# Optimization experiments

Measured on AMD Instinct MI355X. Metric: run time of the kernel, lower is better.

The kernel has to match this reference:

```python
import jax, jax.numpy as jnp
from jax import lax
import numpy as np

B, T, K = 256, 1024, 128


def setup_inputs() -> dict:
    key = jax.random.key(0)
    k1, k2, k3 = jax.random.split(key, 3)
    inputs = jax.random.normal(k1, (B, T, K), dtype=jnp.float32)
    transitions = jax.random.normal(k2, (K, K), dtype=jnp.float32)
    tags = jax.random.randint(k3, (B, T), 0, K, dtype=jnp.int64)
    mask = jnp.ones((B, T), dtype=jnp.int32)
    return {"inputs": inputs, "transitions": transitions, "tags": tags, "mask": mask}


def _input_likelihood(inputs, transitions, maskf):
    # inputs: [B,T,K] emissions; forward algorithm (no start/end transitions)
    emit = jnp.transpose(inputs, (1, 0, 2))  # [T,B,K]
    m = jnp.transpose(maskf, (1, 0))         # [T,B]
    alpha0 = emit[0]                          # [B,K]

    def step(alpha, xm):
        e, mi = xm  # e: [B,K], mi: [B]
        # inner[b,i,j] = alpha[b,i] + transitions[i,j] + e[b,j]
        inner = alpha[:, :, None] + transitions[None, :, :] + e[:, None, :]
        new = jax.nn.logsumexp(inner, axis=1)  # [B,K]
        alpha = new * mi[:, None] + alpha * (1.0 - mi[:, None])
        return alpha, None

    alpha, _ = lax.scan(step, alpha0, (emit[1:], m[1:]))
    return jax.nn.logsumexp(alpha, axis=-1)  # [B]


def _joint_likelihood(inputs, transitions, tags, mask, maskf):
    b, t, k = inputs.shape
    # transition scores between consecutive gold tags
    trans_scores = transitions[tags[:, :-1], tags[:, 1:]]              # [B,T-1]
    # emission scores at gold tags
    emit_scores = jnp.take_along_axis(inputs, tags[..., None], axis=2)[..., 0]  # [B,T]
    score = jnp.sum(trans_scores * maskf[:, 1:], axis=-1) \
          + jnp.sum(emit_scores[:, :-1] * maskf[:, :-1], axis=-1)
    # last valid tag's emission at the final timestep (AllenNLP semantics)
    last_idx = jnp.sum(mask, axis=1).astype(jnp.int32) - 1             # [B]
    last_tags = jnp.take_along_axis(tags, last_idx[:, None].astype(tags.dtype), axis=1)[:, 0]
    last_input_score = jnp.take_along_axis(inputs[:, -1, :], last_tags[:, None], axis=1)[:, 0]
    score = score + last_input_score * maskf[:, -1]
    return score  # [B]


def reference(inputs, transitions, tags, mask):
    maskf = mask.astype(inputs.dtype)
    log_denominator = _input_likelihood(inputs, transitions, maskf)
    log_numerator = _joint_likelihood(inputs, transitions, tags, mask, maskf)
    loglik = log_numerator - log_denominator
    return jnp.sum(loglik)  # reduction='sum'
```

## Files before the change

kernel.cpp:

```cpp
#include <hip/hip_runtime.h>
#include <math.h>

#define BB 256
#define TT 1024
#define KK 128
#define NTHR 512
#define CHUNK 16
#define NCHUNK (TT / CHUNK)
#define QSTR 40

__global__ void zero_out_kernel(float* out) { out[0] = 0.0f; }

#define LOBF(u) __uint_as_float((u) << 16)
#define HIBF(u) __uint_as_float((u) & 0xFFFF0000u)

#define LDE(V, I0) { V.x = expf(tcol[(size_t)(I0) * KK]); \
                     V.y = expf(tcol[(size_t)((I0) + 1) * KK]); \
                     V.z = expf(tcol[(size_t)((I0) + 2) * KK]); \
                     V.w = expf(tcol[(size_t)((I0) + 3) * KK]); }

#define FMA8(V, EA, EB) { \
    z0 = fmaf(LOBF(V.x), EA.x, z0); z1 = fmaf(HIBF(V.x), EA.y, z1); \
    z2 = fmaf(LOBF(V.y), EA.z, z2); z3 = fmaf(HIBF(V.y), EA.w, z3); \
    z0 = fmaf(LOBF(V.z), EB.x, z0); z1 = fmaf(HIBF(V.z), EB.y, z1); \
    z2 = fmaf(LOBF(V.w), EB.z, z2); z3 = fmaf(HIBF(V.w), EB.w, z3); }

#define BARSYNC() { asm volatile("s_waitcnt lgkmcnt(0)" ::: "memory"); \
                    __builtin_amdgcn_s_barrier(); \
                    asm volatile("" ::: "memory"); }

__global__ __launch_bounds__(NTHR, 2) void crf_kernel(
    const float* __restrict__ inputs,
    const float* __restrict__ trans,
    const int* __restrict__ tags,
    const int* __restrict__ mask,
    float* __restrict__ out)
{
    __shared__ __align__(16) unsigned short pbuf[2][4 * QSTR];
    __shared__ __align__(16) float ebuf[2][CHUNK * KK];
    __shared__ float mbuf[2][CHUNK];
    __shared__ float scratch[16];

    const int tid = threadIdx.x;
    const int q   = tid & 3;
    const int j   = tid >> 2;
    const int b   = blockIdx.x;

    const float* binp = inputs + (size_t)b * TT * KK;
    const int* bmask  = mask + (size_t)b * TT;
    const int* btags  = tags + (size_t)b * TT;

    const float* tcol = trans + j;
    const int ib = q * 32;
    float4 E0, E1, E2, E3, E4, E5, E6, E7;
    LDE(E0, ib + 0)  LDE(E1, ib + 4)
    LDE(E2, ib + 8)  LDE(E3, ib + 12)
    LDE(E4, ib + 16) LDE(E5, ib + 20)
    LDE(E6, ib + 24) LDE(E7, ib + 28)

    {
        float4 e4 = ((const float4*)binp)[tid];
        e4.x = __expf(e4.x); e4.y = __expf(e4.y);
        e4.z = __expf(e4.z); e4.w = __expf(e4.w);
        ((float4*)ebuf[0])[tid] = e4;
    }
    if (tid < CHUNK) mbuf[0][tid] = (float)bmask[tid];
    BARSYNC();

    float pcur = ebuf[0][j];
    int m_int = 0;
    if (q == 0) {
        unsigned bits = __float_as_uint(pcur);
        unsigned r = (bits + 0x7FFFu + ((bits >> 16) & 1u)) >> 16;
        pbuf[0][(j >> 5) * QSTR + (j & 31)] = (unsigned short)r;
    }
    BARSYNC();

    for (int c = 0; c < NCHUNK; ++c) {
        float4 epre; int mpre = 0;
        if (c + 1 < NCHUNK) {
            epre = ((const float4*)(binp + (size_t)(c + 1) * CHUNK * KK))[tid];
            if (tid < CHUNK) mpre = bmask[(c + 1) * CHUNK + tid];
        }
        const float* eb = ebuf[c & 1];
        const float* mb = mbuf[c & 1];
        const int s0 = (c == 0) ? 1 : 0;
        for (int s = s0; s < CHUNK; ++s) {
            const int t = c * CHUNK + s;
            const uint4* pr4 = (const uint4*)(pbuf[(t - 1) & 1] + q * QSTR);
            uint4 v0 = pr4[0], v1 = pr4[1], v2 = pr4[2], v3 = pr4[3];
            float z0 = 0.f, z1 = 0.f, z2 = 0.f, z3 = 0.f;
            FMA8(v0, E0, E1) FMA8(v1, E2, E3)
            FMA8(v2, E4, E5) FMA8(v3, E6, E7)
            float z = (z0 + z1) + (z2 + z3);
            z += __shfl_xor(z, 1);
            z += __shfl_xor(z, 2);
            float X  = eb[s * KK + j];
            float mi = mb[s];
            float pn = (mi != 0.0f) ? z * X : pcur;
            unsigned u0 = v0.x << 16;
            int Ex = (int)((u0 >> 23) & 255u) - 127;
            float sc = __uint_as_float((unsigned)(127 - Ex) << 23);
            pcur = pn * sc;
            m_int += Ex;
            if (q == 0) {
                unsigned bits = __float_as_uint(pcur);
                unsigned r = (bits + 0x7FFFu + ((bits >> 16) & 1u)) >> 16;
                pbuf[t & 1][(j >> 5) * QSTR + (j & 31)] = (unsigned short)r;
            }
            BARSYNC();
        }
        if (c + 1 < NCHUNK) {
            epre.x = __expf(epre.x); epre.y = __expf(epre.y);
            epre.z = __expf(epre.z); epre.w = __expf(epre.w);
            ((float4*)ebuf[(c + 1) & 1])[tid] = epre;
            if (tid < CHUNK) mbuf[(c + 1) & 1][tid] = (float)mpre;
            BARSYNC();
        }
    }

    float a = (q == 0) ? ((float)m_int * 0.69314718055994531f + logf(pcur))
                       : -INFINITY;
    float v = a;
#pragma unroll
    for (int o = 1; o < 64; o <<= 1) v = fmaxf(v, __shfl_xor(v, o));
    if ((tid & 63) == 0) scratch[tid >> 6] = v;
    __syncthreads();
    float mx = fmaxf(fmaxf(fmaxf(scratch[0], scratch[1]), fmaxf(scratch[2], scratch[3])),
                     fmaxf(fmaxf(scratch[4], scratch[5]), fmaxf(scratch[6], scratch[7])));
    float ev = (q == 0) ? __expf(a - mx) : 0.0f;
#pragma unroll
    for (int o = 1; o < 64; o <<= 1) ev += __shfl_xor(ev, o);
    __syncthreads();
    if ((tid & 63) == 0) scratch[tid >> 6] = ev;
    __syncthreads();
    float den = mx + logf(((scratch[0] + scratch[1]) + (scratch[2] + scratch[3]))
                        + ((scratch[4] + scratch[5]) + (scratch[6] + scratch[7])));

    float numpart = 0.0f, maskpart = 0.0f;
#pragma unroll
    for (int kk = 0; kk < TT / NTHR; ++kk) {
        int t = tid + NTHR * kk;
        int tg = btags[t];
        float mf = (float)bmask[t];
        maskpart += mf;
        if (t < TT - 1) {
            int tg1   = btags[t + 1];
            float mf1 = (float)bmask[t + 1];
            numpart += trans[tg * KK + tg1] * mf1;
            numpart += binp[(size_t)t * KK + tg] * mf;
        }
    }
#pragma unroll
    for (int o = 1; o < 64; o <<= 1) numpart += __shfl_xor(numpart, o);
#pragma unroll
    for (int o = 1; o < 64; o <<= 1) maskpart += __shfl_xor(maskpart, o);
    __syncthreads();
    if ((tid & 63) == 0) {
        scratch[tid >> 6]       = numpart;
        scratch[8 + (tid >> 6)] = maskpart;
    }
    __syncthreads();
    if (tid == 0) {
        float num  = ((scratch[0] + scratch[1]) + (scratch[2] + scratch[3]))
                   + ((scratch[4] + scratch[5]) + (scratch[6] + scratch[7]));
        float msum = ((scratch[8] + scratch[9]) + (scratch[10] + scratch[11]))
                   + ((scratch[12] + scratch[13]) + (scratch[14] + scratch[15]));
        int last_idx = (int)msum - 1;
        int ltag = btags[last_idx];
        num += binp[(size_t)(TT - 1) * KK + ltag] * (float)bmask[TT - 1];
        atomicAdd(out, num - den);
    }
}

extern "C" void kernel_launch(void* const* d_in, const int* in_sizes, int n_in,
                              void* d_out, int out_size, void* d_ws, size_t ws_size,
                              hipStream_t stream) {
    const float* inputs = (const float*)d_in[0];
    const float* trans  = (const float*)d_in[1];
    const int* tagsp    = (const int*)d_in[2];
    const int* maskp    = (const int*)d_in[3];
    float* out          = (float*)d_out;
    zero_out_kernel<<<1, 1, 0, stream>>>(out);
    crf_kernel<<<BB, NTHR, 0, stream>>>(inputs, trans, tagsp, maskp, out);
}
```

Baseline: 645.6 us.

## Batch 16 sequences per block and compute forward recurrence with bf16 MFMA

The forward recurrence now processes 16 batch rows per block and does each time step as a 16x128 by 128x128 product using MFMA bf16 instructions. The exp(transitions) matrix is split into hi and lo bf16 parts to keep precision. The numerator is moved into a separate kernel, and the chunk size drops to 4 with a swizzled emission buffer. Only 16 blocks are launched, so the serial 1024-step chain runs on few CUs; per-step latency through MFMA plus a barrier decides the outcome.

Measured after the change: 874.2 us. 35.4% more time.

```diff
diff --git a/kernel.cpp b/kernel.cpp
--- a/kernel.cpp
+++ b/kernel.cpp
@@ -4,143 +4,197 @@
 #define BB 256
 #define TT 1024
 #define KK 128
+#define NB 16
+#define NBLK (BB / NB)
 #define NTHR 512
-#define CHUNK 16
+#define CHUNK 4
 #define NCHUNK (TT / CHUNK)
-#define QSTR 40
+#define PSTR 136
+
+typedef __attribute__((ext_vector_type(8))) short bf16x8;
+typedef __attribute__((ext_vector_type(4))) float f32x4;
 
 __global__ void zero_out_kernel(float* out) { out[0] = 0.0f; }
 
-#define LOBF(u) __uint_as_float((u) << 16)
-#define HIBF(u) __uint_as_float((u) & 0xFFFF0000u)
-
-#define LDE(V, I0) { V.x = expf(tcol[(size_t)(I0) * KK]); \
-                     V.y = expf(tcol[(size_t)((I0) + 1) * KK]); \
-                     V.z = expf(tcol[(size_t)((I0) + 2) * KK]); \
-                     V.w = expf(tcol[(size_t)((I0) + 3) * KK]); }
-
-#define FMA8(V, EA, EB) { \
-    z0 = fmaf(LOBF(V.x), EA.x, z0); z1 = fmaf(HIBF(V.x), EA.y, z1); \
-    z2 = fmaf(LOBF(V.y), EA.z, z2); z3 = fmaf(HIBF(V.y), EA.w, z3); \
-    z0 = fmaf(LOBF(V.z), EB.x, z0); z1 = fmaf(HIBF(V.z), EB.y, z1); \
-    z2 = fmaf(LOBF(V.w), EB.z, z2); z3 = fmaf(HIBF(V.w), EB.w, z3); }
+__device__ __forceinline__ unsigned short f2bf(float x) {
+    unsigned b = __float_as_uint(x);
+    return (unsigned short)((b + 0x7FFFu + ((b >> 16) & 1u)) >> 16);
+}
 
 #define BARSYNC() { asm volatile("s_waitcnt lgkmcnt(0)" ::: "memory"); \
                     __builtin_amdgcn_s_barrier(); \
                     asm volatile("" ::: "memory"); }
 
-__global__ __launch_bounds__(NTHR, 2) void crf_kernel(
+#define XI(S, R, J) (((S) * NB + (R)) * KK + ((((J) >> 2) ^ ((R) & 7)) << 2) + ((J) & 3))
+
+__device__ __forceinline__ void ldb(const float* __restrict__ trans, int kbase, int jc,
+                                    bf16x8& BH, bf16x8& BL) {
+#pragma unroll
+    for (int e = 0; e < 8; ++e) {
+        float v = expf(trans[(size_t)(kbase + e) * KK + jc]);
+        unsigned short hb = f2bf(v);
+        float hv = __uint_as_float(((unsigned)hb) << 16);
+        BH[e] = (short)hb;
+        BL[e] = (short)f2bf(v - hv);
+    }
+}
+
+__global__ __launch_bounds__(NTHR, 1) void crf_fwd(
+    const float* __restrict__ inputs,
+    const float* __restrict__ trans,
+    const int* __restrict__ mask,
+    float* __restrict__ out)
+{
+    __shared__ __align__(16) unsigned short pbuf[2][NB * PSTR];
+    __shared__ __align__(16) float ebuf[2][CHUNK * NB * KK];
+    __shared__ float mbuf[2][CHUNK * NB];
+
+    const int tid = threadIdx.x;
+    const int l   = tid & 63;
+    const int w   = tid >> 6;
+    const int jc  = w * 16 + (l & 15);
+    const int kg  = l >> 4;
+    const int r0  = kg * 4;
+    const int b0  = blockIdx.x * NB;
+
+    const int bb = tid >> 5;
+    const int kq = tid & 31;
+    const float* sbase = inputs + (size_t)(b0 + bb) * TT * KK + (size_t)kq * 4;
+    const int xw = ((kq ^ (bb & 7)) << 2);
+
+    bf16x8 Bh0, Bh1, Bh2, Bh3, Bl0, Bl1, Bl2, Bl3;
+    ldb(trans,  0 + kg * 8, jc, Bh0, Bl0);
+    ldb(trans, 32 + kg * 8, jc, Bh1, Bl1);
+    ldb(trans, 64 + kg * 8, jc, Bh2, Bl2);
+    ldb(trans, 96 + kg * 8, jc, Bh3, Bl3);
+
+#pragma unroll
+    for (int s = 0; s < CHUNK; ++s) {
+        float4 e4 = *(const float4*)(sbase + (size_t)s * KK);
+        e4.x = __expf(e4.x); e4.y = __expf(e4.y);
+        e4.z = __expf(e4.z); e4.w = __expf(e4.w);
+        *(float4*)&ebuf[0][(s * NB + bb) * KK + xw] = e4;
+    }
+    if (tid < CHUNK * NB) {
+        int s = tid >> 4, bq = tid & 15;
+        mbuf[0][s * NB + bq] = (float)mask[(size_t)(b0 + bq) * TT + s];
+    }
+    BARSYNC();
+
+    float pcur0, pcur1, pcur2, pcur3;
+    int m0 = 0, m1 = 0, m2 = 0, m3 = 0;
+    pcur0 = ebuf[0][XI(0, r0 + 0, jc)];
+    pcur1 = ebuf[0][XI(0, r0 + 1, jc)];
+    pcur2 = ebuf[0][XI(0, r0 + 2, jc)];
+    pcur3 = ebuf[0][XI(0, r0 + 3, jc)];
+    pbuf[0][(r0 + 0) * PSTR + jc] = f2bf(pcur0);
+    pbuf[0][(r0 + 1) * PSTR + jc] = f2bf(pcur1);
+    pbuf[0][(r0 + 2) * PSTR + jc] = f2bf(pcur2);
+    pbuf[0][(r0 + 3) * PSTR + jc] = f2bf(pcur3);
+    BARSYNC();
+
+#define KSTEP(KT, BH, BL) { \
+    union { uint4 q; bf16x8 v; } _a; \
+    _a.q = *(const uint4*)(Pp + abase0 + (KT) * 32); \
+    acch = __builtin_amdgcn_mfma_f32_16x16x32_bf16(_a.v, BH, acch, 0, 0, 0); \
+    accl = __builtin_amdgcn_mfma_f32_16x16x32_bf16(_a.v, BL, accl, 0, 0, 0); }
+
+#define EPI(I, PC, MI, UU) { \
+    float z = acch[I] + accl[I]; \
+    float X = eb[XI(s, r0 + I, jc)]; \
+    float mi = mb[s * NB + r0 + I]; \
+    int Ex = (int)((UU >> 7) & 255u) - 127; \
+    float sc = __uint_as_float((unsigned)(127 - Ex) << 23); \
+    float pn = (mi != 0.0f) ? z * X : PC; \
+    PC = pn * sc; \
+    MI += Ex; \
+    Pn[(r0 + I) * PSTR + jc] = f2bf(PC); }
+
+    const int abase0 = (l & 15) * PSTR + kg * 8;
+
+    for (int c = 0; c < NCHUNK; ++c) {
+        float4 pf0, pf1, pf2, pf3; int mpre = 0;
+        if (c + 1 < NCHUNK) {
+            const float* pb_ = sbase + (size_t)(c + 1) * CHUNK * KK;
+            pf0 = *(const float4*)(pb_ + 0 * KK);
+            pf1 = *(const float4*)(pb_ + 1 * KK);
+            pf2 = *(const float4*)(pb_ + 2 * KK);
+            pf3 = *(const float4*)(pb_ + 3 * KK);
+            if (tid < CHUNK * NB)
+                mpre = mask[(size_t)(b0 + (tid & 15)) * TT + (c + 1) * CHUNK + (tid >> 4)];
+        }
+        const float* eb = ebuf[c & 1];
+        const float* mb = mbuf[c & 1];
+        for (int s = (c == 0) ? 1 : 0; s < CHUNK; ++s) {
+            const int t = c * CHUNK + s;
+            const unsigned short* Pp = pbuf[(t - 1) & 1];
+            unsigned short* Pn = pbuf[t & 1];
+            f32x4 acch = {0.f, 0.f, 0.f, 0.f};
+            f32x4 accl = {0.f, 0.f, 0.f, 0.f};
+            KSTEP(0, Bh0, Bl0) KSTEP(1, Bh1, Bl1)
+            KSTEP(2, Bh2, Bl2) KSTEP(3, Bh3, Bl3)
+            unsigned short u0 = Pp[(r0 + 0) * PSTR];
+            unsigned short u1 = Pp[(r0 + 1) * PSTR];
+            unsigned short u2 = Pp[(r0 + 2) * PSTR];
+            unsigned short u3 = Pp[(r0 + 3) * PSTR];
+            EPI(0, pcur0, m0, u0) EPI(1, pcur1, m1, u1)
+            EPI(2, pcur2, m2, u2) EPI(3, pcur3, m3, u3)
+            BARSYNC();
+        }
+        if (c + 1 < NCHUNK) {
+            float* en = ebuf[(c + 1) & 1];
+            pf0.x = __expf(pf0.x); pf0.y = __expf(pf0.y); pf0.z = __expf(pf0.z); pf0.w = __expf(pf0.w);
+            pf1.x = __expf(pf1.x); pf1.y = __expf(pf1.y); pf1.z = __expf(pf1.z); pf1.w = __expf(pf1.w);
+            pf2.x = __expf(pf2.x); pf2.y = __expf(pf2.y); pf2.z = __expf(pf2.z); pf2.w = __expf(pf2.w);
+            pf3.x = __expf(pf3.x); pf3.y = __expf(pf3.y); pf3.z = __expf(pf3.z); pf3.w = __expf(pf3.w);
+            *(float4*)&en[(0 * NB + bb) * KK + xw] = pf0;
+            *(float4*)&en[(1 * NB + bb) * KK + xw] = pf1;
+            *(float4*)&en[(2 * NB + bb) * KK + xw] = pf2;
+            *(float4*)&en[(3 * NB + bb) * KK + xw] = pf3;
+            if (tid < CHUNK * NB)
+                mbuf[(c + 1) & 1][(tid >> 4) * NB + (tid & 15)] = (float)mpre;
+            BARSYNC();
+        }
+    }
+
+    float* aw = ebuf[0];
+    aw[(r0 + 0) * KK + jc] = (float)m0 * 0.69314718055994531f + logf(pcur0);
+    aw[(r0 + 1) * KK + jc] = (float)m1 * 0.69314718055994531f + logf(pcur1);
+    aw[(r0 + 2) * KK + jc] = (float)m2 * 0.69314718055994531f + logf(pcur2);
+    aw[(r0 + 3) * KK + jc] = (float)m3 * 0.69314718055994531f + logf(pcur3);
+    BARSYNC();
+    {
+        int bq = tid >> 5, l32 = tid & 31;
+        const float* ab = aw + bq * KK;
+        float a0 = ab[l32 * 4 + 0], a1 = ab[l32 * 4 + 1];
+        float a2 = ab[l32 * 4 + 2], a3 = ab[l32 * 4 + 3];
+        float mx = fmaxf(fmaxf(a0, a1), fmaxf(a2, a3));
+#pragma unroll
+        for (int o = 1; o < 32; o <<= 1) mx = fmaxf(mx, __shfl_xor(mx, o));
+        float ev = __expf(a0 - mx) + __expf(a1 - mx) + __expf(a2 - mx) + __expf(a3 - mx);
+#pragma unroll
+        for (int o = 1; o < 32; o <<= 1) ev += __shfl_xor(ev, o);
+        if (l32 == 0) atomicAdd(out, -(mx + logf(ev)));
+    }
+}
+
+__global__ __launch_bounds__(256, 1) void crf_num(
     const float* __restrict__ inputs,
     const float* __restrict__ trans,
     const int* __restrict__ tags,
     const int* __restrict__ mask,
     float* __restrict__ out)
 {
-    __shared__ __align__(16) unsigned short pbuf[2][4 * QSTR];
-    __shared__ __align__(16) float ebuf[2][CHUNK * KK];
-    __shared__ float mbuf[2][CHUNK];
-    __shared__ float scratch[16];
-
+    __shared__ float scratch[8];
     const int tid = threadIdx.x;
-    const int q   = tid & 3;
-    const int j   = tid >> 2;
-    const int b   = blockIdx.x;
-
+    const int b = blockIdx.x;
     const float* binp = inputs + (size_t)b * TT * KK;
     const int* bmask  = mask + (size_t)b * TT;
     const int* btags  = tags + (size_t)b * TT;
-
-    const float* tcol = trans + j;
-    const int ib = q * 32;
-    float4 E0, E1, E2, E3, E4, E5, E6, E7;
-    LDE(E0, ib + 0)  LDE(E1, ib + 4)
-    LDE(E2, ib + 8)  LDE(E3, ib + 12)
-    LDE(E4, ib + 16) LDE(E5, ib + 20)
-    LDE(E6, ib + 24) LDE(E7, ib + 28)
-
-    {
-        float4 e4 = ((const float4*)binp)[tid];
-        e4.x = __expf(e4.x); e4.y = __expf(e4.y);
-        e4.z = __expf(e4.z); e4.w = __expf(e4.w);
-        ((float4*)ebuf[0])[tid] = e4;
-    }
-    if (tid < CHUNK) mbuf[0][tid] = (float)bmask[tid];
-    BARSYNC();
-
-    float pcur = ebuf[0][j];
-    int m_int = 0;
-    if (q == 0) {
-        unsigned bits = __float_as_uint(pcur);
-        unsigned r = (bits + 0x7FFFu + ((bits >> 16) & 1u)) >> 16;
-        pbuf[0][(j >> 5) * QSTR + (j & 31)] = (unsigned short)r;
-    }
-    BARSYNC();
-
-    for (int c = 0; c < NCHUNK; ++c) {
-        float4 epre; int mpre = 0;
-        if (c + 1 < NCHUNK) {
-            epre = ((const float4*)(binp + (size_t)(c + 1) * CHUNK * KK))[tid];
-            if (tid < CHUNK) mpre = bmask[(c + 1) * CHUNK + tid];
-        }
-        const float* eb = ebuf[c & 1];
-        const float* mb = mbuf[c & 1];
-        const int s0 = (c == 0) ? 1 : 0;
-        for (int s = s0; s < CHUNK; ++s) {
-            const int t = c * CHUNK + s;
-            const uint4* pr4 = (const uint4*)(pbuf[(t - 1) & 1] + q * QSTR);
-            uint4 v0 = pr4[0], v1 = pr4[1], v2 = pr4[2], v3 = pr4[3];
-            float z0 = 0.f, z1 = 0.f, z2 = 0.f, z3 = 0.f;
-            FMA8(v0, E0, E1) FMA8(v1, E2, E3)
-            FMA8(v2, E4, E5) FMA8(v3, E6, E7)
-            float z = (z0 + z1) + (z2 + z3);
-            z += __shfl_xor(z, 1);
-            z += __shfl_xor(z, 2);
-            float X  = eb[s * KK + j];
-            float mi = mb[s];
-            float pn = (mi != 0.0f) ? z * X : pcur;
-            unsigned u0 = v0.x << 16;
-            int Ex = (int)((u0 >> 23) & 255u) - 127;
-            float sc = __uint_as_float((unsigned)(127 - Ex) << 23);
-            pcur = pn * sc;
-            m_int += Ex;
-            if (q == 0) {
-                unsigned bits = __float_as_uint(pcur);
-                unsigned r = (bits + 0x7FFFu + ((bits >> 16) & 1u)) >> 16;
-                pbuf[t & 1][(j >> 5) * QSTR + (j & 31)] = (unsigned short)r;
-            }
-            BARSYNC();
-        }
-        if (c + 1 < NCHUNK) {
-            epre.x = __expf(epre.x); epre.y = __expf(epre.y);
-            epre.z = __expf(epre.z); epre.w = __expf(epre.w);
-            ((float4*)ebuf[(c + 1) & 1])[tid] = epre;
-            if (tid < CHUNK) mbuf[(c + 1) & 1][tid] = (float)mpre;
-            BARSYNC();
-        }
-    }
-
-    float a = (q == 0) ? ((float)m_int * 0.69314718055994531f + logf(pcur))
-                       : -INFINITY;
-    float v = a;
-#pragma unroll
-    for (int o = 1; o < 64; o <<= 1) v = fmaxf(v, __shfl_xor(v, o));
-    if ((tid & 63) == 0) scratch[tid >> 6] = v;
-    __syncthreads();
-    float mx = fmaxf(fmaxf(fmaxf(scratch[0], scratch[1]), fmaxf(scratch[2], scratch[3])),
-                     fmaxf(fmaxf(scratch[4], scratch[5]), fmaxf(scratch[6], scratch[7])));
-    float ev = (q == 0) ? __expf(a - mx) : 0.0f;
-#pragma unroll
-    for (int o = 1; o < 64; o <<= 1) ev += __shfl_xor(ev, o);
-    __syncthreads();
-    if ((tid & 63) == 0) scratch[tid >> 6] = ev;
-    __syncthreads();
-    float den = mx + logf(((scratch[0] + scratch[1]) + (scratch[2] + scratch[3]))
-                        + ((scratch[4] + scratch[5]) + (scratch[6] + scratch[7])));
-
     float numpart = 0.0f, maskpart = 0.0f;
 #pragma unroll
-    for (int kk = 0; kk < TT / NTHR; ++kk) {
-        int t = tid + NTHR * kk;
+    for (int kk2 = 0; kk2 < TT / 256; ++kk2) {
+        int t = tid + 256 * kk2;
         int tg = btags[t];
         float mf = (float)bmask[t];
         maskpart += mf;
@@ -155,21 +209,18 @@
     for (int o = 1; o < 64; o <<= 1) numpart += __shfl_xor(numpart, o);
 #pragma unroll
     for (int o = 1; o < 64; o <<= 1) maskpart += __shfl_xor(maskpart, o);
-    __syncthreads();
     if ((tid & 63) == 0) {
-        scratch[tid >> 6]       = numpart;
-        scratch[8 + (tid >> 6)] = maskpart;
+        scratch[tid >> 6]     = numpart;
+        scratch[4 + (tid >> 6)] = maskpart;
     }
     __syncthreads();
     if (tid == 0) {
-        float num  = ((scratch[0] + scratch[1]) + (scratch[2] + scratch[3]))
-                   + ((scratch[4] + scratch[5]) + (scratch[6] + scratch[7]));
-        float msum = ((scratch[8] + scratch[9]) + (scratch[10] + scratch[11]))
-                   + ((scratch[12] + scratch[13]) + (scratch[14] + scratch[15]));
+        float num  = (scratch[0] + scratch[1]) + (scratch[2] + scratch[3]);
+        float msum = (scratch[4] + scratch[5]) + (scratch[6] + scratch[7]);
         int last_idx = (int)msum - 1;
         int ltag = btags[last_idx];
         num += binp[(size_t)(TT - 1) * KK + ltag] * (float)bmask[TT - 1];
-        atomicAdd(out, num - den);
+        atomicAdd(out, num);
     }
 }
 
@@ -182,5 +233,6 @@
     const int* maskp    = (const int*)d_in[3];
     float* out          = (float*)d_out;
     zero_out_kernel<<<1, 1, 0, stream>>>(out);
-    crf_kernel<<<BB, NTHR, 0, stream>>>(inputs, trans, tagsp, maskp, out);
-}
+    crf_num<<<BB, 256, 0, stream>>>(inputs, trans, tagsp, maskp, out);
+    crf_fwd<<<NBLK, NTHR, 0, stream>>>(inputs, trans, maskp, out);
+}
```

## Use 1024-thread blocks with fp32 probability buffer and periodic rescaling

Applied to the files above, without the earlier changes.

Doubles the block to 1024 threads, with 8 threads per output tag each doing a 16-element dot product instead of 4 threads each doing 32. The bf16-packed probability buffer becomes plain fp32 in shared memory, and exponent renormalisation now runs every 4 steps instead of every step. The intent is to shorten the per-step serial dot-product latency in the recurrence. In exchange it adds a third shuffle stage, a barrier across 16 wavefronts per step, and one block per CU instead of two.

Result: slower. 756.6 us (+17.2%).

```diff
diff --git a/kernel.cpp b/kernel.cpp
--- a/kernel.cpp
+++ b/kernel.cpp
@@ -4,59 +4,45 @@
 #define BB 256
 #define TT 1024
 #define KK 128
-#define NTHR 512
-#define CHUNK 16
+#define NTHR 1024
+#define CHUNK 32
 #define NCHUNK (TT / CHUNK)
-#define QSTR 40
 
 __global__ void zero_out_kernel(float* out) { out[0] = 0.0f; }
-
-#define LOBF(u) __uint_as_float((u) << 16)
-#define HIBF(u) __uint_as_float((u) & 0xFFFF0000u)
-
-#define LDE(V, I0) { V.x = expf(tcol[(size_t)(I0) * KK]); \
-                     V.y = expf(tcol[(size_t)((I0) + 1) * KK]); \
-                     V.z = expf(tcol[(size_t)((I0) + 2) * KK]); \
-                     V.w = expf(tcol[(size_t)((I0) + 3) * KK]); }
-
-#define FMA8(V, EA, EB) { \
-    z0 = fmaf(LOBF(V.x), EA.x, z0); z1 = fmaf(HIBF(V.x), EA.y, z1); \
-    z2 = fmaf(LOBF(V.y), EA.z, z2); z3 = fmaf(HIBF(V.y), EA.w, z3); \
-    z0 = fmaf(LOBF(V.z), EB.x, z0); z1 = fmaf(HIBF(V.z), EB.y, z1); \
-    z2 = fmaf(LOBF(V.w), EB.z, z2); z3 = fmaf(HIBF(V.w), EB.w, z3); }
 
 #define BARSYNC() { asm volatile("s_waitcnt lgkmcnt(0)" ::: "memory"); \
                     __builtin_amdgcn_s_barrier(); \
                     asm volatile("" ::: "memory"); }
 
-__global__ __launch_bounds__(NTHR, 2) void crf_kernel(
+__global__ __launch_bounds__(NTHR, 1) void crf_kernel(
     const float* __restrict__ inputs,
     const float* __restrict__ trans,
     const int* __restrict__ tags,
     const int* __restrict__ mask,
     float* __restrict__ out)
 {
-    __shared__ __align__(16) unsigned short pbuf[2][4 * QSTR];
-    __shared__ __align__(16) float ebuf[2][CHUNK * KK];
+    __shared__ __align__(16) float pbuf[2][KK];
+    __shared__ __align__(16) float ebuf[2][CHUNK*KK];
     __shared__ float mbuf[2][CHUNK];
-    __shared__ float scratch[16];
+    __shared__ float scratch[32];
 
     const int tid = threadIdx.x;
-    const int q   = tid & 3;
-    const int j   = tid >> 2;
+    const int j   = tid >> 3;
+    const int q   = tid & 7;
     const int b   = blockIdx.x;
 
     const float* binp = inputs + (size_t)b * TT * KK;
     const int* bmask  = mask + (size_t)b * TT;
     const int* btags  = tags + (size_t)b * TT;
 
-    const float* tcol = trans + j;
-    const int ib = q * 32;
-    float4 E0, E1, E2, E3, E4, E5, E6, E7;
-    LDE(E0, ib + 0)  LDE(E1, ib + 4)
-    LDE(E2, ib + 8)  LDE(E3, ib + 12)
-    LDE(E4, ib + 16) LDE(E5, ib + 20)
-    LDE(E6, ib + 24) LDE(E7, ib + 28)
+    float4 E0, E1, E2, E3;
+    {
+        const float* tc = trans + (size_t)(q * 16) * KK + j;
+        E0.x = expf(tc[0*KK]);  E0.y = expf(tc[1*KK]);  E0.z = expf(tc[2*KK]);  E0.w = expf(tc[3*KK]);
+        E1.x = expf(tc[4*KK]);  E1.y = expf(tc[5*KK]);  E1.z = expf(tc[6*KK]);  E1.w = expf(tc[7*KK]);
+        E2.x = expf(tc[8*KK]);  E2.y = expf(tc[9*KK]);  E2.z = expf(tc[10*KK]); E2.w = expf(tc[11*KK]);
+        E3.x = expf(tc[12*KK]); E3.y = expf(tc[13*KK]); E3.z = expf(tc[14*KK]); E3.w = expf(tc[15*KK]);
+    }
 
     {
         float4 e4 = ((const float4*)binp)[tid];
@@ -69,11 +55,7 @@
 
     float pcur = ebuf[0][j];
     int m_int = 0;
-    if (q == 0) {
-        unsigned bits = __float_as_uint(pcur);
-        unsigned r = (bits + 0x7FFFu + ((bits >> 16) & 1u)) >> 16;
-        pbuf[0][(j >> 5) * QSTR + (j & 31)] = (unsigned short)r;
-    }
+    if (q == 0) pbuf[0][j] = pcur;
     BARSYNC();
 
     for (int c = 0; c < NCHUNK; ++c) {
@@ -84,30 +66,35 @@
         }
         const float* eb = ebuf[c & 1];
         const float* mb = mbuf[c & 1];
-        const int s0 = (c == 0) ? 1 : 0;
-        for (int s = s0; s < CHUNK; ++s) {
+        for (int s = (c == 0) ? 1 : 0; s < CHUNK; ++s) {
             const int t = c * CHUNK + s;
-            const uint4* pr4 = (const uint4*)(pbuf[(t - 1) & 1] + q * QSTR);
-            uint4 v0 = pr4[0], v1 = pr4[1], v2 = pr4[2], v3 = pr4[3];
-            float z0 = 0.f, z1 = 0.f, z2 = 0.f, z3 = 0.f;
-            FMA8(v0, E0, E1) FMA8(v1, E2, E3)
-            FMA8(v2, E4, E5) FMA8(v3, E6, E7)
+            const float* Pp = pbuf[(t - 1) & 1];
+            const float4* pr = (const float4*)(Pp + q * 16);
+            float4 p0 = pr[0], p1 = pr[1], p2 = pr[2], p3 = pr[3];
+            float z0 = p0.x * E0.x; z0 = fmaf(p0.y, E0.y, z0);
+            z0 = fmaf(p0.z, E0.z, z0); z0 = fmaf(p0.w, E0.w, z0);
+            float z1 = p1.x * E1.x; z1 = fmaf(p1.y, E1.y, z1);
+            z1 = fmaf(p1.z, E1.z, z1); z1 = fmaf(p1.w, E1.w, z1);
+            float z2 = p2.x * E2.x; z2 = fmaf(p2.y, E2.y, z2);
+            z2 = fmaf(p2.z, E2.z, z2); z2 = fmaf(p2.w, E2.w, z2);
+            float z3 = p3.x * E3.x; z3 = fmaf(p3.y, E3.y, z3);
+            z3 = fmaf(p3.z, E3.z, z3); z3 = fmaf(p3.w, E3.w, z3);
             float z = (z0 + z1) + (z2 + z3);
             z += __shfl_xor(z, 1);
             z += __shfl_xor(z, 2);
+            z += __shfl_xor(z, 4);
             float X  = eb[s * KK + j];
             float mi = mb[s];
             float pn = (mi != 0.0f) ? z * X : pcur;
-            unsigned u0 = v0.x << 16;
-            int Ex = (int)((u0 >> 23) & 255u) - 127;
-            float sc = __uint_as_float((unsigned)(127 - Ex) << 23);
-            pcur = pn * sc;
-            m_int += Ex;
-            if (q == 0) {
-                unsigned bits = __float_as_uint(pcur);
-                unsigned r = (bits + 0x7FFFu + ((bits >> 16) & 1u)) >> 16;
-                pbuf[t & 1][(j >> 5) * QSTR + (j & 31)] = (unsigned short)r;
+            if ((s & 3) == 3) {
+                unsigned u = __float_as_uint(Pp[0]);
+                int Ex = (int)((u >> 23) & 255u) - 127;
+                float sc = __uint_as_float((unsigned)(127 - Ex) << 23);
+                pn *= sc;
+                m_int += Ex;
             }
+            pcur = pn;
+            if (q == 0) pbuf[t & 1][j] = pn;
             BARSYNC();
         }
         if (c + 1 < NCHUNK) {
@@ -119,53 +106,45 @@
         }
     }
 
-    float a = (q == 0) ? ((float)m_int * 0.69314718055994531f + logf(pcur))
-                       : -INFINITY;
-    float v = a;
+    float* aw = ebuf[0];
+    if (q == 0) aw[j] = (float)m_int * 0.69314718055994531f + logf(pcur);
+    BARSYNC();
+    float den = 0.0f;
+    if (tid < 64) {
+        float a0 = aw[tid], a1 = aw[tid + 64];
+        float mx = fmaxf(a0, a1);
 #pragma unroll
-    for (int o = 1; o < 64; o <<= 1) v = fmaxf(v, __shfl_xor(v, o));
-    if ((tid & 63) == 0) scratch[tid >> 6] = v;
-    __syncthreads();
-    float mx = fmaxf(fmaxf(fmaxf(scratch[0], scratch[1]), fmaxf(scratch[2], scratch[3])),
-                     fmaxf(fmaxf(scratch[4], scratch[5]), fmaxf(scratch[6], scratch[7])));
-    float ev = (q == 0) ? __expf(a - mx) : 0.0f;
+        for (int o = 1; o < 64; o <<= 1) mx = fmaxf(mx, __shfl_xor(mx, o));
+        float ev = __expf(a0 - mx) + __expf(a1 - mx);
 #pragma unroll
-    for (int o = 1; o < 64; o <<= 1) ev += __shfl_xor(ev, o);
-    __syncthreads();
-    if ((tid & 63) == 0) scratch[tid >> 6] = ev;
-    __syncthreads();
-    float den = mx + logf(((scratch[0] + scratch[1]) + (scratch[2] + scratch[3]))
-                        + ((scratch[4] + scratch[5]) + (scratch[6] + scratch[7])));
+        for (int o = 1; o < 64; o <<= 1) ev += __shfl_xor(ev, o);
+        den = mx + logf(ev);
+    }
 
     float numpart = 0.0f, maskpart = 0.0f;
-#pragma unroll
-    for (int kk = 0; kk < TT / NTHR; ++kk) {
-        int t = tid + NTHR * kk;
+    {
+        int t = tid;
         int tg = btags[t];
         float mf = (float)bmask[t];
-        maskpart += mf;
+        maskpart = mf;
         if (t < TT - 1) {
-            int tg1   = btags[t + 1];
-            float mf1 = (float)bmask[t + 1];
-            numpart += trans[tg * KK + tg1] * mf1;
-            numpart += binp[(size_t)t * KK + tg] * mf;
+            numpart = trans[tg * KK + btags[t + 1]] * (float)bmask[t + 1]
+                    + binp[(size_t)t * KK + tg] * mf;
         }
     }
 #pragma unroll
-    for (int o = 1; o < 64; o <<= 1) numpart += __shfl_xor(numpart, o);
+    for (int o = 1; o < 64; o <<= 1) numpart  += __shfl_xor(numpart, o);
 #pragma unroll
     for (int o = 1; o < 64; o <<= 1) maskpart += __shfl_xor(maskpart, o);
-    __syncthreads();
     if ((tid & 63) == 0) {
-        scratch[tid >> 6]       = numpart;
-        scratch[8 + (tid >> 6)] = maskpart;
+        scratch[tid >> 6]      = numpart;
+        scratch[16 + (tid >> 6)] = maskpart;
     }
-    __syncthreads();
+    BARSYNC();
     if (tid == 0) {
-        float num  = ((scratch[0] + scratch[1]) + (scratch[2] + scratch[3]))
-                   + ((scratch[4] + scratch[5]) + (scratch[6] + scratch[7]));
-        float msum = ((scratch[8] + scratch[9]) + (scratch[10] + scratch[11]))
-                   + ((scratch[12] + scratch[13]) + (scratch[14] + scratch[15]));
+        float num = 0.0f, msum = 0.0f;
+#pragma unroll
+        for (int k2 = 0; k2 < 16; ++k2) { num += scratch[k2]; msum += scratch[16 + k2]; }
         int last_idx = (int)msum - 1;
         int ltag = btags[last_idx];
         num += binp[(size_t)(TT - 1) * KK + ltag] * (float)bmask[TT - 1];
```
